# Optimization experiments

Hardware: AMD Instinct MI355X
Metric: run time of the kernel (lower is better)

Reference implementation:

```python
import jax, jax.numpy as jnp
import numpy as np

N_NODES = 100000
N_EDGES = 600000
DIM = 128          # node feature dim == hidden_dim == output_dim
NUM_HEADS = 4
HEAD_DIM = DIM // NUM_HEADS


def setup_inputs() -> dict:
    key = jax.random.key(0)
    ks = jax.random.split(key, 8)
    s = 1.0 / np.sqrt(DIM).astype(np.float32)
    nodes = jax.random.normal(ks[0], (N_NODES, DIM), jnp.float32)
    senders = jax.random.randint(ks[1], (N_EDGES,), 0, N_NODES, jnp.int32)
    receivers = jax.random.randint(ks[2], (N_EDGES,), 0, N_NODES, jnp.int32)
    Wq = jax.random.normal(ks[3], (DIM, DIM), jnp.float32) * s
    Wk = jax.random.normal(ks[4], (DIM, DIM), jnp.float32) * s
    Wv = jax.random.normal(ks[5], (DIM, DIM), jnp.float32) * s
    Wo = jax.random.normal(ks[6], (DIM, DIM), jnp.float32) * s
    bq = jnp.zeros((DIM,), jnp.float32)
    bk = jnp.zeros((DIM,), jnp.float32)
    bv = jnp.zeros((DIM,), jnp.float32)
    bo = jnp.zeros((DIM,), jnp.float32)
    return {"nodes": nodes, "senders": senders, "receivers": receivers,
            "Wq": Wq, "bq": bq, "Wk": Wk, "bk": bk,
            "Wv": Wv, "bv": bv, "Wo": Wo, "bo": bo}


def reference(nodes, senders, receivers, Wq, bq, Wk, bk, Wv, bv, Wo, bo):
    N = nodes.shape[0]
    inv_sqrt_hd = jnp.float32(1.0 / np.sqrt(HEAD_DIM))
    # Q/K/V projections, reshaped to [N, H, hd]
    q = (nodes @ Wq + bq).reshape(N, NUM_HEADS, HEAD_DIM)
    k = (nodes @ Wk + bk).reshape(N, NUM_HEADS, HEAD_DIM)
    v = (nodes @ Wv + bv).reshape(N, NUM_HEADS, HEAD_DIM)
    # Gather per edge: [E, H, hd]
    q_s = q[senders]
    k_r = k[receivers]
    scores = jnp.sum(q_s * k_r, axis=-1) * inv_sqrt_hd  # [E, H]
    # NOTE: faithful to source -- softmax is over the HEADS axis, not neighbors
    attn = jax.nn.softmax(scores, axis=-1)              # [E, H]
    weighted = (v[senders] * attn[:, :, None]).reshape(-1, DIM)  # [E, DIM]
    aggregated = jax.ops.segment_sum(weighted, receivers, num_segments=N)  # [N, DIM]
    out = aggregated @ Wo + bo
    # residual: nodes.shape[-1] == output_dim
    return out + nodes
```

## Files before the change

kernel.cpp:

```cpp
#include <hip/hip_runtime.h>
#include <hip/hip_bf16.h>

#define N_DIM 128
#define NHEADS 4
#define HEAD_DIM 32

typedef unsigned short bf16_t;
typedef short bf16x8 __attribute__((ext_vector_type(8)));
typedef float f32x4 __attribute__((ext_vector_type(4)));

__device__ __forceinline__ float bf16_to_f32(unsigned int u16) {
    union { unsigned int i; float f; } x;
    x.i = u16 << 16;
    return x.f;
}

__device__ __forceinline__ float lof(unsigned int u) {
    union { unsigned int i; float f; } x; x.i = u << 16; return x.f;
}
__device__ __forceinline__ float hif(unsigned int u) {
    union { unsigned int i; float f; } x; x.i = u & 0xffff0000u; return x.f;
}

__device__ __forceinline__ bf16_t f32_to_bf16(float f) {
    union { float f; unsigned int i; } x;
    x.f = f;
    unsigned int r = x.i + 0x7FFFu + ((x.i >> 16) & 1u);
    return (bf16_t)(r >> 16);
}

#define LDA_STRIDE 136

__global__ __launch_bounds__(128) void transpose_w_kernel(
    const float* __restrict__ Wq, const float* __restrict__ Wk,
    const float* __restrict__ Wv, const float* __restrict__ Wo,
    bf16_t* __restrict__ Wt, bf16_t* __restrict__ Wot)
{
    const int n = blockIdx.x;
    const int k = threadIdx.x;
    const float* W; bf16_t* dst; int nl;
    if (n < 128)      { W = Wq; nl = n;       dst = Wt  + n * 128; }
    else if (n < 256) { W = Wk; nl = n - 128; dst = Wt  + n * 128; }
    else if (n < 384) { W = Wv; nl = n - 256; dst = Wt  + n * 128; }
    else              { W = Wo; nl = n - 384; dst = Wot + (n - 384) * 128; }
    dst[k] = f32_to_bf16(W[k * 128 + nl]);
}

__global__ __launch_bounds__(256) void qkv_mfma_kernel(
    const float* __restrict__ nodes,
    const bf16_t* __restrict__ Wt,
    const float* __restrict__ bq, const float* __restrict__ bk,
    const float* __restrict__ bv,
    bf16_t* __restrict__ qb, bf16_t* __restrict__ kb, bf16_t* __restrict__ vb,
    int N)
{
    __shared__ bf16_t lds_a[32 * LDA_STRIDE];
    const int tid = threadIdx.x;
    const int m0 = blockIdx.x * 32;

#pragma unroll
    for (int i = 0; i < 4; ++i) {
        const int f = tid + 256 * i;
        const int row = f >> 5, c4 = f & 31;
        const int g = m0 + row;
        float4 v = make_float4(0.f, 0.f, 0.f, 0.f);
        if (g < N) v = ((const float4*)nodes)[(size_t)g * 32 + c4];
        ushort4 u;
        u.x = f32_to_bf16(v.x); u.y = f32_to_bf16(v.y);
        u.z = f32_to_bf16(v.z); u.w = f32_to_bf16(v.w);
        *(ushort4*)(lds_a + row * LDA_STRIDE + c4 * 4) = u;
    }
    __syncthreads();

    const int w  = tid >> 6;
    const int l  = tid & 63;
    const int lr = l & 15;
    const int lg = l >> 4;

    bf16x8 a[2][4];
#pragma unroll
    for (int mt = 0; mt < 2; ++mt)
#pragma unroll
        for (int kt = 0; kt < 4; ++kt)
            a[mt][kt] = *(const bf16x8*)(lds_a + (mt * 16 + lr) * LDA_STRIDE
                                         + kt * 32 + lg * 8);

#pragma unroll
    for (int ni = 0; ni < 6; ++ni) {
        const int nt = w * 6 + ni;
        f32x4 acc0 = {0.f, 0.f, 0.f, 0.f};
        f32x4 acc1 = {0.f, 0.f, 0.f, 0.f};
#pragma unroll
        for (int kt = 0; kt < 4; ++kt) {
            const bf16x8 b = *(const bf16x8*)(Wt + (size_t)(nt * 16 + lr) * 128
                                              + kt * 32 + lg * 8);
            acc0 = __builtin_amdgcn_mfma_f32_16x16x32_bf16(b, a[0][kt], acc0, 0, 0, 0);
            acc1 = __builtin_amdgcn_mfma_f32_16x16x32_bf16(b, a[1][kt], acc1, 0, 0, 0);
        }
        const int fb = nt * 16 + lg * 4;
        bf16_t* dst; int cl; const float* bias;
        if (nt < 8)       { dst = qb; cl = fb;       bias = bq; }
        else if (nt < 16) { dst = kb; cl = fb - 128; bias = bk; }
        else              { dst = vb; cl = fb - 256; bias = bv; }
        const float4 b4 = *(const float4*)(bias + cl);

        uint2 p0, p1;
        p0.x = (unsigned)f32_to_bf16(acc0[0] + b4.x)
             | ((unsigned)f32_to_bf16(acc0[1] + b4.y) << 16);
        p0.y = (unsigned)f32_to_bf16(acc0[2] + b4.z)
             | ((unsigned)f32_to_bf16(acc0[3] + b4.w) << 16);
        p1.x = (unsigned)f32_to_bf16(acc1[0] + b4.x)
             | ((unsigned)f32_to_bf16(acc1[1] + b4.y) << 16);
        p1.y = (unsigned)f32_to_bf16(acc1[2] + b4.z)
             | ((unsigned)f32_to_bf16(acc1[3] + b4.w) << 16);

        const int r0 = m0 + lr;
        const int r1 = m0 + 16 + lr;
        if (r0 < N) *(uint2*)(dst + (size_t)r0 * 128 + cl) = p0;
        if (r1 < N) *(uint2*)(dst + (size_t)r1 * 128 + cl) = p1;
    }
}

__global__ __launch_bounds__(256) void hist_kernel(
    const int* __restrict__ receivers, int* __restrict__ cnt, int E)
{
    const int i = blockIdx.x * 256 + threadIdx.x;
    if (i < E) atomicAdd(&cnt[receivers[i]], 1);
}

__global__ __launch_bounds__(256) void scan_block_kernel(
    const int* __restrict__ cnt, int* __restrict__ starts,
    int* __restrict__ bsum, int N)
{
    __shared__ int sc[256];
    const int t = threadIdx.x;
    const int base = blockIdx.x * 1024 + t * 4;
    int v0 = (base + 0 < N) ? cnt[base + 0] : 0;
    int v1 = (base + 1 < N) ? cnt[base + 1] : 0;
    int v2 = (base + 2 < N) ? cnt[base + 2] : 0;
    int v3 = (base + 3 < N) ? cnt[base + 3] : 0;
    const int s = v0 + v1 + v2 + v3;
    sc[t] = s;
    __syncthreads();
    for (int off = 1; off < 256; off <<= 1) {
        int x = (t >= off) ? sc[t - off] : 0;
        __syncthreads();
        sc[t] += x;
        __syncthreads();
    }
    int excl = sc[t] - s;
    if (base + 0 < N) starts[base + 0] = excl;
    if (base + 1 < N) starts[base + 1] = excl + v0;
    if (base + 2 < N) starts[base + 2] = excl + v0 + v1;
    if (base + 3 < N) starts[base + 3] = excl + v0 + v1 + v2;
    if (t == 255) bsum[blockIdx.x] = sc[255];
}

__global__ __launch_bounds__(256) void scan_top_kernel(
    const int* __restrict__ bsum, int* __restrict__ boff,
    int* __restrict__ starts, int nb, int N)
{
    __shared__ int sc[256];
    const int t = threadIdx.x;
    const int s = (t < nb) ? bsum[t] : 0;
    sc[t] = s;
    __syncthreads();
    for (int off = 1; off < 256; off <<= 1) {
        int x = (t >= off) ? sc[t - off] : 0;
        __syncthreads();
        sc[t] += x;
        __syncthreads();
    }
    if (t < nb) boff[t] = sc[t] - s;
    if (t == 255) starts[N] = sc[255];
}

__global__ __launch_bounds__(256) void scan_add_kernel(
    int* __restrict__ starts, int* __restrict__ cursor,
    const int* __restrict__ boff, int N)
{
    const int t = threadIdx.x;
    const int base = blockIdx.x * 1024 + t * 4;
    const int o = boff[blockIdx.x];
#pragma unroll
    for (int k = 0; k < 4; ++k) {
        const int i = base + k;
        if (i < N) {
            const int v = starts[i] + o;
            starts[i] = v;
            cursor[i] = v;
        }
    }
}

__global__ __launch_bounds__(256) void scatter_kernel(
    const int* __restrict__ senders, const int* __restrict__ receivers,
    int* __restrict__ cursor, int* __restrict__ elist, int E)
{
    const int i = blockIdx.x * 256 + threadIdx.x;
    if (i < E) {
        const int pos = atomicAdd(&cursor[receivers[i]], 1);
        elist[pos] = senders[i];
    }
}

__global__ __launch_bounds__(256) void agg_kernel(
    const int* __restrict__ starts, const int* __restrict__ elist,
    const bf16_t* __restrict__ qb, const bf16_t* __restrict__ kb,
    const bf16_t* __restrict__ vb,
    bf16_t* __restrict__ agg_b, int N)
{
    const int r = blockIdx.x * 4 + (threadIdx.x >> 6);
    const int lane = threadIdx.x & 63;
    if (r >= N) return;

    const int start = starts[r];
    const int end   = starts[r + 1];
    const int c = lane * 2;

    const unsigned int ku = *(const unsigned int*)(kb + (size_t)r * N_DIM + c);
    const float kx = lof(ku), ky = hif(ku);

    float ax = 0.f, ay = 0.f;
    const float scale = 0.17677669529663687f;
    const int h = lane >> 4;

    for (int j0 = start; j0 < end; j0 += 64) {
        const int ids = (j0 + lane < end) ? elist[j0 + lane] : 0;
        const int jm = min(64, end - j0);
        for (int j = 0; j < jm; ++j) {
            const int s = __shfl(ids, j);
            const unsigned int qu =
                *(const unsigned int*)(qb + (size_t)s * N_DIM + c);
            const unsigned int vu =
                *(const unsigned int*)(vb + (size_t)s * N_DIM + c);
            const float qx = lof(qu), qy = hif(qu);

            float p = qx * kx + qy * ky;
            p += __shfl_xor(p, 1);
            p += __shfl_xor(p, 2);
            p += __shfl_xor(p, 4);
            p += __shfl_xor(p, 8);

            const float s0 = __shfl(p, 0)  * scale;
            const float s1 = __shfl(p, 16) * scale;
            const float s2 = __shfl(p, 32) * scale;
            const float s3 = __shfl(p, 48) * scale;

            const float m = fmaxf(fmaxf(s0, s1), fmaxf(s2, s3));
            const float e0 = __expf(s0 - m);
            const float e1 = __expf(s1 - m);
            const float e2 = __expf(s2 - m);
            const float e3 = __expf(s3 - m);
            const float inv = 1.0f / (e0 + e1 + e2 + e3);
            const float aw = (h == 0 ? e0 : h == 1 ? e1 : h == 2 ? e2 : e3) * inv;

            ax = fmaf(lof(vu), aw, ax);
            ay = fmaf(hif(vu), aw, ay);
        }
    }

    const unsigned int packed =
        (unsigned int)f32_to_bf16(ax) | ((unsigned int)f32_to_bf16(ay) << 16);
    *(unsigned int*)(agg_b + (size_t)r * N_DIM + c) = packed;
}

__global__ __launch_bounds__(256) void out_mfma_b_kernel(
    const float* __restrict__ nodes,
    const bf16_t* __restrict__ agg_b,
    const bf16_t* __restrict__ Wot,
    const float* __restrict__ bo,
    float* __restrict__ out, int N)
{
    __shared__ bf16_t lds_a[32 * LDA_STRIDE];
    const int tid = threadIdx.x;
    const int m0 = blockIdx.x * 32;

#pragma unroll
    for (int i = 0; i < 4; ++i) {
        const int f = tid + 256 * i;
        const int row = f >> 5, c4 = f & 31;
        const int g = m0 + row;
        ushort4 u = make_ushort4(0, 0, 0, 0);
        if (g < N) u = ((const ushort4*)(agg_b + (size_t)g * N_DIM))[c4];
        *(ushort4*)(lds_a + row * LDA_STRIDE + c4 * 4) = u;
    }
    __syncthreads();

    const int w  = tid >> 6;
    const int l  = tid & 63;
    const int lr = l & 15;
    const int lg = l >> 4;

    bf16x8 a[2][4];
#pragma unroll
    for (int mt = 0; mt < 2; ++mt)
#pragma unroll
        for (int kt = 0; kt < 4; ++kt)
            a[mt][kt] = *(const bf16x8*)(lds_a + (mt * 16 + lr) * LDA_STRIDE
                                         + kt * 32 + lg * 8);

#pragma unroll
    for (int ni = 0; ni < 2; ++ni) {
        const int nt = w * 2 + ni;
        f32x4 acc0 = {0.f, 0.f, 0.f, 0.f};
        f32x4 acc1 = {0.f, 0.f, 0.f, 0.f};
#pragma unroll
        for (int kt = 0; kt < 4; ++kt) {
            const bf16x8 b = *(const bf16x8*)(Wot + (size_t)(nt * 16 + lr) * 128
                                              + kt * 32 + lg * 8);
            acc0 = __builtin_amdgcn_mfma_f32_16x16x32_bf16(b, a[0][kt], acc0, 0, 0, 0);
            acc1 = __builtin_amdgcn_mfma_f32_16x16x32_bf16(b, a[1][kt], acc1, 0, 0, 0);
        }
        const int fb = nt * 16 + lg * 4;
        const float4 b4 = *(const float4*)(bo + fb);

        const int r0 = m0 + lr;
        const int r1 = m0 + 16 + lr;
        if (r0 < N) {
            const float4 nd = *(const float4*)(nodes + (size_t)r0 * 128 + fb);
            float4 res;
            res.x = acc0[0] + b4.x + nd.x;
            res.y = acc0[1] + b4.y + nd.y;
            res.z = acc0[2] + b4.z + nd.z;
            res.w = acc0[3] + b4.w + nd.w;
            *(float4*)(out + (size_t)r0 * 128 + fb) = res;
        }
        if (r1 < N) {
            const float4 nd = *(const float4*)(nodes + (size_t)r1 * 128 + fb);
            float4 res;
            res.x = acc1[0] + b4.x + nd.x;
            res.y = acc1[1] + b4.y + nd.y;
            res.z = acc1[2] + b4.z + nd.z;
            res.w = acc1[3] + b4.w + nd.w;
            *(float4*)(out + (size_t)r1 * 128 + fb) = res;
        }
    }
}

__global__ __launch_bounds__(256) void edge_kernel(
    const int* __restrict__ senders, const int* __restrict__ receivers,
    const bf16_t* __restrict__ qb, const bf16_t* __restrict__ kb,
    const bf16_t* __restrict__ vb,
    float* __restrict__ agg, int E)
{
    const int wid = threadIdx.x >> 6;
    const int lane = threadIdx.x & 63;
    const int e = blockIdx.x * 4 + wid;
    if (e >= E) return;

    const int s = senders[e];
    const int r = receivers[e];

    const int c = lane * 2;
    const unsigned int qu = *(const unsigned int*)(qb + (size_t)s * N_DIM + c);
    const unsigned int ku = *(const unsigned int*)(kb + (size_t)r * N_DIM + c);
    const unsigned int vu = *(const unsigned int*)(vb + (size_t)s * N_DIM + c);

    const float qx = lof(qu), qy = hif(qu);
    const float kx = lof(ku), ky = hif(ku);

    float p = qx * kx + qy * ky;
    p += __shfl_xor(p, 1);
    p += __shfl_xor(p, 2);
    p += __shfl_xor(p, 4);
    p += __shfl_xor(p, 8);

    const float scale = 0.17677669529663687f;
    const float s0 = __shfl(p, 0)  * scale;
    const float s1 = __shfl(p, 16) * scale;
    const float s2 = __shfl(p, 32) * scale;
    const float s3 = __shfl(p, 48) * scale;

    const float m = fmaxf(fmaxf(s0, s1), fmaxf(s2, s3));
    const float e0 = __expf(s0 - m);
    const float e1 = __expf(s1 - m);
    const float e2 = __expf(s2 - m);
    const float e3 = __expf(s3 - m);
    const float inv = 1.0f / (e0 + e1 + e2 + e3);

    const int h = lane >> 4;
    const float aw = (h == 0 ? e0 : h == 1 ? e1 : h == 2 ? e2 : e3) * inv;

    const float wx = lof(vu) * aw;
    const float wy = hif(vu) * aw;

    float* dst = agg + (size_t)r * N_DIM + c;
    atomicAdd(dst, wx);
    atomicAdd(dst + 1, wy);
}

__global__ __launch_bounds__(256) void out_mfma_kernel(
    const float* __restrict__ nodes,
    const bf16_t* __restrict__ Wot,
    const float* __restrict__ bo,
    float* __restrict__ out, int N)
{
    __shared__ bf16_t lds_a[32 * LDA_STRIDE];
    const int tid = threadIdx.x;
    const int m0 = blockIdx.x * 32;

#pragma unroll
    for (int i = 0; i < 4; ++i) {
        const int f = tid + 256 * i;
        const int row = f >> 5, c4 = f & 31;
        const int g = m0 + row;
        float4 v = make_float4(0.f, 0.f, 0.f, 0.f);
        if (g < N) v = ((const float4*)out)[(size_t)g * 32 + c4];
        ushort4 u;
        u.x = f32_to_bf16(v.x); u.y = f32_to_bf16(v.y);
        u.z = f32_to_bf16(v.z); u.w = f32_to_bf16(v.w);
        *(ushort4*)(lds_a + row * LDA_STRIDE + c4 * 4) = u;
    }
    __syncthreads();

    const int w  = tid >> 6;
    const int l  = tid & 63;
    const int lr = l & 15;
    const int lg = l >> 4;

    bf16x8 a[2][4];
#pragma unroll
    for (int mt = 0; mt < 2; ++mt)
#pragma unroll
        for (int kt = 0; kt < 4; ++kt)
            a[mt][kt] = *(const bf16x8*)(lds_a + (mt * 16 + lr) * LDA_STRIDE
                                         + kt * 32 + lg * 8);

#pragma unroll
    for (int ni = 0; ni < 2; ++ni) {
        const int nt = w * 2 + ni;
        const int col = nt * 16 + lr;
        f32x4 acc0 = {0.f, 0.f, 0.f, 0.f};
        f32x4 acc1 = {0.f, 0.f, 0.f, 0.f};
#pragma unroll
        for (int kt = 0; kt < 4; ++kt) {
            const bf16x8 b = *(const bf16x8*)(Wot + (size_t)col * 128
                                              + kt * 32 + lg * 8);
            acc0 = __builtin_amdgcn_mfma_f32_16x16x32_bf16(a[0][kt], b, acc0, 0, 0, 0);
            acc1 = __builtin_amdgcn_mfma_f32_16x16x32_bf16(a[1][kt], b, acc1, 0, 0, 0);
        }
        const float bb = bo[col];
#pragma unroll
        for (int j = 0; j < 4; ++j) {
            const int r0 = m0 + lg * 4 + j;
            if (r0 < N)
                out[(size_t)r0 * 128 + col] =
                    acc0[j] + bb + nodes[(size_t)r0 * 128 + col];
            const int r1 = m0 + 16 + lg * 4 + j;
            if (r1 < N)
                out[(size_t)r1 * 128 + col] =
                    acc1[j] + bb + nodes[(size_t)r1 * 128 + col];
        }
    }
}

extern "C" void kernel_launch(void* const* d_in, const int* in_sizes, int n_in,
                              void* d_out, int out_size, void* d_ws, size_t ws_size,
                              hipStream_t stream)
{
    const float* nodes   = (const float*)d_in[0];
    const int* senders   = (const int*)d_in[1];
    const int* receivers = (const int*)d_in[2];
    const float* Wq = (const float*)d_in[3];
    const float* bq = (const float*)d_in[4];
    const float* Wk = (const float*)d_in[5];
    const float* bk = (const float*)d_in[6];
    const float* Wv = (const float*)d_in[7];
    const float* bv = (const float*)d_in[8];
    const float* Wo = (const float*)d_in[9];
    const float* bo = (const float*)d_in[10];

    const int N = in_sizes[0] / N_DIM;
    const int E = in_sizes[1];

    float* out = (float*)d_out;
    char* ws = (char*)d_ws;

    const size_t row_bytes = (size_t)N * N_DIM * sizeof(bf16_t);
    size_t off = 0;
    bf16_t* qb    = (bf16_t*)(ws + off); off += row_bytes;
    bf16_t* kb    = (bf16_t*)(ws + off); off += row_bytes;
    bf16_t* vb    = (bf16_t*)(ws + off); off += row_bytes;
    bf16_t* Wt    = (bf16_t*)(ws + off); off += 384 * 128 * sizeof(bf16_t);
    bf16_t* Wot   = (bf16_t*)(ws + off); off += 128 * 128 * sizeof(bf16_t);
    bf16_t* agg_b = (bf16_t*)(ws + off); off += row_bytes;
    int* cnt      = (int*)(ws + off);    off += (size_t)N * 4;
    int* starts   = (int*)(ws + off);    off += (size_t)(N + 1) * 4;
    int* cursor   = (int*)(ws + off);    off += (size_t)N * 4;
    int* elist    = (int*)(ws + off);    off += (size_t)E * 4;
    int* bsum     = (int*)(ws + off);    off += 256 * 4;
    int* boff     = (int*)(ws + off);    off += 256 * 4;
    const size_t need_csr = off;
    const size_t need_mid = 3 * row_bytes + (384 + 128) * 128 * sizeof(bf16_t);

    const int nb = (N + 1023) / 1024;

    if (ws_size >= need_csr && nb <= 256) {
        transpose_w_kernel<<<512, 128, 0, stream>>>(Wq, Wk, Wv, Wo, Wt, Wot);
        qkv_mfma_kernel<<<(N + 31) / 32, 256, 0, stream>>>(
            nodes, Wt, bq, bk, bv, qb, kb, vb, N);

        hipMemsetAsync(cnt, 0, (size_t)N * 4, stream);
        hist_kernel<<<(E + 255) / 256, 256, 0, stream>>>(receivers, cnt, E);
        scan_block_kernel<<<nb, 256, 0, stream>>>(cnt, starts, bsum, N);
        scan_top_kernel<<<1, 256, 0, stream>>>(bsum, boff, starts, nb, N);
        scan_add_kernel<<<nb, 256, 0, stream>>>(starts, cursor, boff, N);
        scatter_kernel<<<(E + 255) / 256, 256, 0, stream>>>(
            senders, receivers, cursor, elist, E);

        agg_kernel<<<(N + 3) / 4, 256, 0, stream>>>(
            starts, elist, qb, kb, vb, agg_b, N);

        out_mfma_b_kernel<<<(N + 31) / 32, 256, 0, stream>>>(
            nodes, agg_b, Wot, bo, out, N);
    } else if (ws_size >= need_mid) {
        hipMemsetAsync(d_out, 0, (size_t)N * N_DIM * sizeof(float), stream);
        transpose_w_kernel<<<512, 128, 0, stream>>>(Wq, Wk, Wv, Wo, Wt, Wot);
        qkv_mfma_kernel<<<(N + 31) / 32, 256, 0, stream>>>(
            nodes, Wt, bq, bk, bv, qb, kb, vb, N);
        edge_kernel<<<(E + 3) / 4, 256, 0, stream>>>(
            senders, receivers, qb, kb, vb, out, E);
        out_mfma_kernel<<<(N + 31) / 32, 256, 0, stream>>>(
            nodes, Wot, bo, out, N);
    }
}
```

Measured before the change: 347.0 us.

## Use 16-lane-per-node aggregation and single-block scan for CSR build

```diff
diff --git a/kernel.cpp b/kernel.cpp
--- a/kernel.cpp
+++ b/kernel.cpp
@@ -8,12 +8,6 @@
 typedef unsigned short bf16_t;
 typedef short bf16x8 __attribute__((ext_vector_type(8)));
 typedef float f32x4 __attribute__((ext_vector_type(4)));
-
-__device__ __forceinline__ float bf16_to_f32(unsigned int u16) {
-    union { unsigned int i; float f; } x;
-    x.i = u16 << 16;
-    return x.f;
-}
 
 __device__ __forceinline__ float lof(unsigned int u) {
     union { unsigned int i; float f; } x; x.i = u << 16; return x.f;
@@ -27,6 +21,10 @@
     x.f = f;
     unsigned int r = x.i + 0x7FFFu + ((x.i >> 16) & 1u);
     return (bf16_t)(r >> 16);
+}
+
+__device__ __forceinline__ unsigned int pack2(float a, float b) {
+    return (unsigned int)f32_to_bf16(a) | ((unsigned int)f32_to_bf16(b) << 16);
 }
 
 #define LDA_STRIDE 136
@@ -105,14 +103,10 @@
         const float4 b4 = *(const float4*)(bias + cl);
 
         uint2 p0, p1;
-        p0.x = (unsigned)f32_to_bf16(acc0[0] + b4.x)
-             | ((unsigned)f32_to_bf16(acc0[1] + b4.y) << 16);
-        p0.y = (unsigned)f32_to_bf16(acc0[2] + b4.z)
-             | ((unsigned)f32_to_bf16(acc0[3] + b4.w) << 16);
-        p1.x = (unsigned)f32_to_bf16(acc1[0] + b4.x)
-             | ((unsigned)f32_to_bf16(acc1[1] + b4.y) << 16);
-        p1.y = (unsigned)f32_to_bf16(acc1[2] + b4.z)
-             | ((unsigned)f32_to_bf16(acc1[3] + b4.w) << 16);
+        p0.x = pack2(acc0[0] + b4.x, acc0[1] + b4.y);
+        p0.y = pack2(acc0[2] + b4.z, acc0[3] + b4.w);
+        p1.x = pack2(acc1[0] + b4.x, acc1[1] + b4.y);
+        p1.y = pack2(acc1[2] + b4.z, acc1[3] + b4.w);
 
         const int r0 = m0 + lr;
         const int r1 = m0 + 16 + lr;
@@ -128,68 +122,40 @@
     if (i < E) atomicAdd(&cnt[receivers[i]], 1);
 }
 
-__global__ __launch_bounds__(256) void scan_block_kernel(
+__global__ __launch_bounds__(1024) void scan_all_kernel(
     const int* __restrict__ cnt, int* __restrict__ starts,
-    int* __restrict__ bsum, int N)
-{
-    __shared__ int sc[256];
+    int* __restrict__ cursor, int N)
+{
+    __shared__ int wsum[16];
+    __shared__ int woff[16];
     const int t = threadIdx.x;
-    const int base = blockIdx.x * 1024 + t * 4;
-    int v0 = (base + 0 < N) ? cnt[base + 0] : 0;
-    int v1 = (base + 1 < N) ? cnt[base + 1] : 0;
-    int v2 = (base + 2 < N) ? cnt[base + 2] : 0;
-    int v3 = (base + 3 < N) ? cnt[base + 3] : 0;
-    const int s = v0 + v1 + v2 + v3;
-    sc[t] = s;
+    const int wid = t >> 6, lane = t & 63;
+    const int chunk = (N + 1023) >> 10;
+    const int b0 = t * chunk;
+    const int b1 = min(b0 + chunk, N);
+
+    int s = 0;
+    for (int i = b0; i < b1; ++i) s += cnt[i];
+    const int my = s;
+
+    for (int off = 1; off < 64; off <<= 1) {
+        int x = __shfl_up(s, off);
+        if (lane >= off) s += x;
+    }
+    if (lane == 63) wsum[wid] = s;
     __syncthreads();
-    for (int off = 1; off < 256; off <<= 1) {
-        int x = (t >= off) ? sc[t - off] : 0;
-        __syncthreads();
-        sc[t] += x;
-        __syncthreads();
-    }
-    int excl = sc[t] - s;
-    if (base + 0 < N) starts[base + 0] = excl;
-    if (base + 1 < N) starts[base + 1] = excl + v0;
-    if (base + 2 < N) starts[base + 2] = excl + v0 + v1;
-    if (base + 3 < N) starts[base + 3] = excl + v0 + v1 + v2;
-    if (t == 255) bsum[blockIdx.x] = sc[255];
-}
-
-__global__ __launch_bounds__(256) void scan_top_kernel(
-    const int* __restrict__ bsum, int* __restrict__ boff,
-    int* __restrict__ starts, int nb, int N)
-{
-    __shared__ int sc[256];
-    const int t = threadIdx.x;
-    const int s = (t < nb) ? bsum[t] : 0;
-    sc[t] = s;
+    if (t == 0) {
+        int run = 0;
+        for (int w = 0; w < 16; ++w) { woff[w] = run; run += wsum[w]; }
+        starts[N] = run;
+    }
     __syncthreads();
-    for (int off = 1; off < 256; off <<= 1) {
-        int x = (t >= off) ? sc[t - off] : 0;
-        __syncthreads();
-        sc[t] += x;
-        __syncthreads();
-    }
-    if (t < nb) boff[t] = sc[t] - s;
-    if (t == 255) starts[N] = sc[255];
-}
-
-__global__ __launch_bounds__(256) void scan_add_kernel(
-    int* __restrict__ starts, int* __restrict__ cursor,
-    const int* __restrict__ boff, int N)
-{
-    const int t = threadIdx.x;
-    const int base = blockIdx.x * 1024 + t * 4;
-    const int o = boff[blockIdx.x];
-#pragma unroll
-    for (int k = 0; k < 4; ++k) {
-        const int i = base + k;
-        if (i < N) {
-            const int v = starts[i] + o;
-            starts[i] = v;
-            cursor[i] = v;
-        }
+
+    int run = s - my + woff[wid];
+    for (int i = b0; i < b1; ++i) {
+        starts[i] = run;
+        cursor[i] = run;
+        run += cnt[i];
     }
 }
 
@@ -202,6 +168,78 @@
         const int pos = atomicAdd(&cursor[receivers[i]], 1);
         elist[pos] = senders[i];
     }
+}
+
+__global__ __launch_bounds__(256) void agg16_kernel(
+    const int* __restrict__ starts, const int* __restrict__ elist,
+    const bf16_t* __restrict__ qb, const bf16_t* __restrict__ kb,
+    const bf16_t* __restrict__ vb,
+    bf16_t* __restrict__ agg_b, int N)
+{
+    const int r = blockIdx.x * 16 + (threadIdx.x >> 4);
+    const int l16 = threadIdx.x & 15;
+    if (r >= N) return;
+
+    const int sbase = threadIdx.x & 0x30;
+    const int h = l16 >> 2;
+    const int start = starts[r];
+    const int end   = starts[r + 1];
+
+    const uint4 ku = *(const uint4*)(kb + (size_t)r * N_DIM + l16 * 8);
+    const float k0 = lof(ku.x), k1 = hif(ku.x), k2 = lof(ku.y), k3 = hif(ku.y);
+    const float k4 = lof(ku.z), k5 = hif(ku.z), k6 = lof(ku.w), k7 = hif(ku.w);
+
+    float a0 = 0.f, a1 = 0.f, a2 = 0.f, a3 = 0.f;
+    float a4 = 0.f, a5 = 0.f, a6 = 0.f, a7 = 0.f;
+    const float scale = 0.17677669529663687f;
+
+    for (int j = start; j < end; ++j) {
+        const int s = elist[j];
+        const uint4 qu = *(const uint4*)(qb + (size_t)s * N_DIM + l16 * 8);
+
+        float p;
+        p = lof(qu.x) * k0;
+        p = fmaf(hif(qu.x), k1, p);
+        p = fmaf(lof(qu.y), k2, p);
+        p = fmaf(hif(qu.y), k3, p);
+        p = fmaf(lof(qu.z), k4, p);
+        p = fmaf(hif(qu.z), k5, p);
+        p = fmaf(lof(qu.w), k6, p);
+        p = fmaf(hif(qu.w), k7, p);
+
+        p += __shfl_xor(p, 1);
+        p += __shfl_xor(p, 2);
+
+        const float s0 = __shfl(p, sbase + 0)  * scale;
+        const float s1 = __shfl(p, sbase + 4)  * scale;
+        const float s2 = __shfl(p, sbase + 8)  * scale;
+        const float s3 = __shfl(p, sbase + 12) * scale;
+
+        const float m = fmaxf(fmaxf(s0, s1), fmaxf(s2, s3));
+        const float e0 = __expf(s0 - m);
+        const float e1 = __expf(s1 - m);
+        const float e2 = __expf(s2 - m);
+        const float e3 = __expf(s3 - m);
+        const float inv = 1.0f / (e0 + e1 + e2 + e3);
+        const float w = (h == 0 ? e0 : h == 1 ? e1 : h == 2 ? e2 : e3) * inv;
+
+        const uint4 vu = *(const uint4*)(vb + (size_t)s * N_DIM + l16 * 8);
+        a0 = fmaf(lof(vu.x), w, a0);
+        a1 = fmaf(hif(vu.x), w, a1);
+        a2 = fmaf(lof(vu.y), w, a2);
+        a3 = fmaf(hif(vu.y), w, a3);
+        a4 = fmaf(lof(vu.z), w, a4);
+        a5 = fmaf(hif(vu.z), w, a5);
+        a6 = fmaf(lof(vu.w), w, a6);
+        a7 = fmaf(hif(vu.w), w, a7);
+    }
+
+    uint4 o;
+    o.x = pack2(a0, a1);
+    o.y = pack2(a2, a3);
+    o.z = pack2(a4, a5);
+    o.w = pack2(a6, a7);
+    *(uint4*)(agg_b + (size_t)r * N_DIM + l16 * 8) = o;
 }
 
 __global__ __launch_bounds__(256) void agg_kernel(
@@ -234,19 +272,15 @@
                 *(const unsigned int*)(qb + (size_t)s * N_DIM + c);
             const unsigned int vu =
                 *(const unsigned int*)(vb + (size_t)s * N_DIM + c);
-            const float qx = lof(qu), qy = hif(qu);
-
-            float p = qx * kx + qy * ky;
+            float p = lof(qu) * kx + hif(qu) * ky;
             p += __shfl_xor(p, 1);
             p += __shfl_xor(p, 2);
             p += __shfl_xor(p, 4);
             p += __shfl_xor(p, 8);
-
             const float s0 = __shfl(p, 0)  * scale;
             const float s1 = __shfl(p, 16) * scale;
             const float s2 = __shfl(p, 32) * scale;
             const float s3 = __shfl(p, 48) * scale;
-
             const float m = fmaxf(fmaxf(s0, s1), fmaxf(s2, s3));
             const float e0 = __expf(s0 - m);
             const float e1 = __expf(s1 - m);
@@ -254,15 +288,11 @@
             const float e3 = __expf(s3 - m);
             const float inv = 1.0f / (e0 + e1 + e2 + e3);
             const float aw = (h == 0 ? e0 : h == 1 ? e1 : h == 2 ? e2 : e3) * inv;
-
             ax = fmaf(lof(vu), aw, ax);
             ay = fmaf(hif(vu), aw, ay);
         }
     }
-
-    const unsigned int packed =
-        (unsigned int)f32_to_bf16(ax) | ((unsigned int)f32_to_bf16(ay) << 16);
-    *(unsigned int*)(agg_b + (size_t)r * N_DIM + c) = packed;
+    *(unsigned int*)(agg_b + (size_t)r * N_DIM + c) = pack2(ax, ay);
 }
 
 __global__ __launch_bounds__(256) void out_mfma_b_kernel(
@@ -357,10 +387,7 @@
     const unsigned int ku = *(const unsigned int*)(kb + (size_t)r * N_DIM + c);
     const unsigned int vu = *(const unsigned int*)(vb + (size_t)s * N_DIM + c);
 
-    const float qx = lof(qu), qy = hif(qu);
-    const float kx = lof(ku), ky = hif(ku);
-
-    float p = qx * kx + qy * ky;
+    float p = lof(qu) * lof(ku) + hif(qu) * hif(ku);
     p += __shfl_xor(p, 1);
     p += __shfl_xor(p, 2);
     p += __shfl_xor(p, 4);
@@ -382,12 +409,9 @@
     const int h = lane >> 4;
     const float aw = (h == 0 ? e0 : h == 1 ? e1 : h == 2 ? e2 : e3) * inv;
 
-    const float wx = lof(vu) * aw;
-    const float wy = hif(vu) * aw;
-
     float* dst = agg + (size_t)r * N_DIM + c;
-    atomicAdd(dst, wx);
-    atomicAdd(dst + 1, wy);
+    atomicAdd(dst, lof(vu) * aw);
+    atomicAdd(dst + 1, hif(vu) * aw);
 }
 
 __global__ __launch_bounds__(256) void out_mfma_kernel(
@@ -489,27 +513,21 @@
     int* starts   = (int*)(ws + off);    off += (size_t)(N + 1) * 4;
     int* cursor   = (int*)(ws + off);    off += (size_t)N * 4;
     int* elist    = (int*)(ws + off);    off += (size_t)E * 4;
-    int* bsum     = (int*)(ws + off);    off += 256 * 4;
-    int* boff     = (int*)(ws + off);    off += 256 * 4;
     const size_t need_csr = off;
     const size_t need_mid = 3 * row_bytes + (384 + 128) * 128 * sizeof(bf16_t);
 
-    const int nb = (N + 1023) / 1024;
-
-    if (ws_size >= need_csr && nb <= 256) {
+    if (ws_size >= need_csr) {
         transpose_w_kernel<<<512, 128, 0, stream>>>(Wq, Wk, Wv, Wo, Wt, Wot);
         qkv_mfma_kernel<<<(N + 31) / 32, 256, 0, stream>>>(
             nodes, Wt, bq, bk, bv, qb, kb, vb, N);
 
         hipMemsetAsync(cnt, 0, (size_t)N * 4, stream);
         hist_kernel<<<(E + 255) / 256, 256, 0, stream>>>(receivers, cnt, E);
-        scan_block_kernel<<<nb, 256, 0, stream>>>(cnt, starts, bsum, N);
-        scan_top_kernel<<<1, 256, 0, stream>>>(bsum, boff, starts, nb, N);
-        scan_add_kernel<<<nb, 256, 0, stream>>>(starts, cursor, boff, N);
+        scan_all_kernel<<<1, 1024, 0, stream>>>(cnt, starts, cursor, N);
         scatter_kernel<<<(E + 255) / 256, 256, 0, stream>>>(
             senders, receivers, cursor, elist, E);
 
-        agg_kernel<<<(N + 3) / 4, 256, 0, stream>>>(
+        agg16_kernel<<<(N + 15) / 16, 256, 0, stream>>>(
             starts, elist, qb, kb, vb, agg_b, N);
 
         out_mfma_b_kernel<<<(N + 31) / 32, 256, 0, stream>>>(
```

Result: slower. 532.3 us (+53.4%).
